# Performance work log

Measured on AMD Instinct MI355X. Metric: run time of the kernel, lower is better.

The kernel has to match this reference:

```python
import jax, jax.numpy as jnp
import numpy as np

DIM = 1024
HIDDEN = 2816  # multiple_of * ceil(int(2*4096/3)/multiple_of)
N_MODALITIES = 2
B, S = 8, 4096


def setup_inputs() -> dict:
    key = jax.random.key(0)
    k_x, k_m, k1, k2, k3 = jax.random.split(key, 5)
    x = jax.random.normal(k_x, (B, S, DIM), dtype=jnp.float32)
    modality_ids = jax.random.randint(k_m, (B, S), 0, N_MODALITIES, dtype=jnp.int32)
    in_std = DIM ** -0.5
    out_std = HIDDEN ** -0.5
    # Linear weight layout: [out_features, in_features], stacked over modalities.
    W1 = jax.random.normal(k1, (N_MODALITIES, HIDDEN, DIM), dtype=jnp.float32) * in_std
    W3 = jax.random.normal(k3, (N_MODALITIES, HIDDEN, DIM), dtype=jnp.float32) * in_std
    W2 = jax.random.normal(k2, (N_MODALITIES, DIM, HIDDEN), dtype=jnp.float32) * out_std
    return {"x": x, "modality_ids": modality_ids, "W1": W1, "W2": W2, "W3": W3}


def reference(x, modality_ids, W1, W2, W3):
    # Masked per-modality SwiGLU; equivalent to gather -> expert MLP -> scatter.
    output = jnp.zeros_like(x)
    for m in range(N_MODALITIES):  # small fixed modality count
        mask = (modality_ids == m)[..., None]          # [B, S, 1]
        x1 = jnp.einsum('bsd,hd->bsh', x, W1[m])       # gate proj
        x3 = jnp.einsum('bsd,hd->bsh', x, W3[m])       # up proj
        out_m = jnp.einsum('bsh,dh->bsd', jax.nn.silu(x1) * x3, W2[m])
        output = output + jnp.where(mask, out_m, 0.0)
    return output
```

## Files before the change

### kernel.cpp

```cpp
#include <hip/hip_runtime.h>
#include <stdint.h>

#define DIMK 1024
#define HID  2816

typedef __attribute__((ext_vector_type(8))) __bf16 bf16x8;
typedef __attribute__((ext_vector_type(4))) float  f32x4;

typedef const __attribute__((address_space(1))) void* gas1_t;
typedef __attribute__((address_space(3))) void*       las3_t;

__device__ __forceinline__ uint16_t f2bf(float f) {
  uint32_t u = __float_as_uint(f);
  u += 0x7FFFu + ((u >> 16) & 1u);
  return (uint16_t)(u >> 16);
}

__device__ __forceinline__ void gload16(const uint16_t* g, uint16_t* l) {
  __builtin_amdgcn_global_load_lds((gas1_t)g, (las3_t)l, 16, 0, 0);
}

template<int N> __device__ __forceinline__ void wait_vm() {
  if constexpr (N == 0)      asm volatile("s_waitcnt vmcnt(0)" ::: "memory");
  else if constexpr (N == 1) asm volatile("s_waitcnt vmcnt(1)" ::: "memory");
  else if constexpr (N == 2) asm volatile("s_waitcnt vmcnt(2)" ::: "memory");
}

__device__ __forceinline__ void stage32(const uint16_t* g, long stride,
                                        uint16_t* lds, int tid) {
  const int row  = tid >> 2;
  const int srcg = (tid & 3) ^ ((tid >> 3) & 3);
  gload16(g + (long)row * stride + srcg * 8, lds + tid * 8);
}

__device__ __forceinline__ bf16x8 ldsf32(const uint16_t* lds, int r, int g) {
  return *reinterpret_cast<const bf16x8*>(lds + r * 32 + ((g ^ ((r >> 1) & 3)) << 3));
}


__global__ void count_kernel(const int* __restrict__ mids, int* __restrict__ bc, int T) {
  const int b = blockIdx.x, t = threadIdx.x;
  const int token = b * 256 + t;
  const int lane = t & 63, wv = t >> 6;
  const int m = (token < T) ? mids[token] : -1;
  unsigned long long m0 = __ballot(m == 0);
  unsigned long long m1 = __ballot(m == 1);
  __shared__ int w0[4], w1[4];
  if (lane == 0) { w0[wv] = __popcll(m0); w1[wv] = __popcll(m1); }
  __syncthreads();
  if (t == 0) {
    bc[2 * b]     = w0[0] + w0[1] + w0[2] + w0[3];
    bc[2 * b + 1] = w1[0] + w1[1] + w1[2] + w1[3];
  }
}

__global__ void scan_kernel(const int* __restrict__ bc, int* __restrict__ base,
                            int* __restrict__ counters, int nb) {
  __shared__ int s0[256], s1[256];
  const int t = threadIdx.x;
  const int v0 = (t < nb) ? bc[2 * t] : 0;
  const int v1 = (t < nb) ? bc[2 * t + 1] : 0;
  s0[t] = v0; s1[t] = v1;
  __syncthreads();
  for (int off = 1; off < 256; off <<= 1) {
    int a0 = (t >= off) ? s0[t - off] : 0;
    int a1 = (t >= off) ? s1[t - off] : 0;
    __syncthreads();
    s0[t] += a0; s1[t] += a1;
    __syncthreads();
  }
  if (t < nb) { base[2 * t] = s0[t] - v0; base[2 * t + 1] = s1[t] - v1; }
  if (t == nb - 1) { counters[0] = s0[t]; counters[1] = s1[t]; }
}

__global__ void slot_kernel(const int* __restrict__ mids, const int* __restrict__ base,
                            const int* __restrict__ counters, int* __restrict__ tok,
                            int* __restrict__ slotof, int T) {
  const int b = blockIdx.x, t = threadIdx.x;
  const int token = b * 256 + t;
  const int lane = t & 63, wv = t >> 6;
  const int m = (token < T) ? mids[token] : -1;
  unsigned long long m0 = __ballot(m == 0);
  unsigned long long m1 = __ballot(m == 1);
  __shared__ int w0[4], w1[4];
  if (lane == 0) { w0[wv] = __popcll(m0); w1[wv] = __popcll(m1); }
  __syncthreads();
  int pre0 = 0, pre1 = 0;
  for (int w = 0; w < wv; ++w) { pre0 += w0[w]; pre1 += w1[w]; }
  if (token >= T) return;
  const unsigned long long below = (1ULL << lane) - 1ULL;
  const int c0 = counters[0];
  const int al0 = ((c0 + 127) >> 7) << 7;
  int slot;
  if (m == 0) slot = base[2 * b] + pre0 + __popcll(m0 & below);
  else        slot = al0 + base[2 * b + 1] + pre1 + __popcll(m1 & below);
  tok[slot] = token;
  slotof[token] = slot;
}

__global__ void copy_kernel(const float* __restrict__ x, const int* __restrict__ slotof,
                            uint16_t* __restrict__ xg, int T) {
  const int token = blockIdx.x * 4 + (threadIdx.x >> 6);
  if (token >= T) return;
  const int lane = threadIdx.x & 63;
  const int slot = slotof[token];
  const float4* src = (const float4*)(x + (long)token * DIMK);
  uint16_t* dst = xg + (long)slot * DIMK;
#pragma unroll
  for (int j = 0; j < 4; ++j) {
    float4 v = src[lane + 64 * j];
    ushort4 o;
    o.x = f2bf(v.x); o.y = f2bf(v.y); o.z = f2bf(v.z); o.w = f2bf(v.w);
    *(ushort4*)(dst + (lane + 64 * j) * 4) = o;
  }
}

__global__ void convert3_kernel(const float* __restrict__ s0, const float* __restrict__ s1,
                                const float* __restrict__ s2, uint16_t* __restrict__ d0,
                                uint16_t* __restrict__ d1, uint16_t* __restrict__ d2,
                                long n, int cblk) {
  const int seg = blockIdx.x / cblk;
  const int bid = blockIdx.x - seg * cblk;
  const float* src = (seg == 0) ? s0 : (seg == 1) ? s1 : s2;
  uint16_t*    dst = (seg == 0) ? d0 : (seg == 1) ? d1 : d2;
  long i = ((long)bid * blockDim.x + threadIdx.x) * 4;
  if (i >= n) return;
  float4 v = *(const float4*)(src + i);
  ushort4 o;
  o.x = f2bf(v.x); o.y = f2bf(v.y); o.z = f2bf(v.z); o.w = f2bf(v.w);
  *(ushort4*)(dst + i) = o;
}


template<bool PF, int W0, int W1>
__device__ __forceinline__ void qt32(
    const uint16_t* Ac, const uint16_t* Bxc, const uint16_t* Byc,
    uint16_t* An, uint16_t* Bxn, uint16_t* Byn,
    const uint16_t* gA, const uint16_t* gBx, const uint16_t* gBy,
    long ko, long stride,
    int tid, int wr, int wc, int lrow, int grp,
    f32x4 (&accX)[4][2], f32x4 (&accY)[4][2]) {
  bf16x8 a[4], bx[2], by[2];
  wait_vm<W0>();
  __builtin_amdgcn_s_barrier();
  asm volatile("" ::: "memory");
#pragma unroll
  for (int m = 0; m < 4; ++m)
    a[m] = ldsf32(Ac, wr * 64 + m * 16 + lrow, grp);
#pragma unroll
  for (int n = 0; n < 2; ++n)
    bx[n] = ldsf32(Bxc, wc * 32 + n * 16 + lrow, grp);
  if constexpr (PF) stage32(gA + ko, stride, An, tid);
  asm volatile("s_waitcnt lgkmcnt(0)" ::: "memory");
  __builtin_amdgcn_sched_barrier(0);
  __builtin_amdgcn_s_setprio(1);
#pragma unroll
  for (int m = 0; m < 4; ++m)
#pragma unroll
    for (int n = 0; n < 2; ++n)
      accX[m][n] = __builtin_amdgcn_mfma_f32_16x16x32_bf16(a[m], bx[n], accX[m][n], 0, 0, 0);
  __builtin_amdgcn_s_setprio(0);
  wait_vm<W1>();
  __builtin_amdgcn_s_barrier();
  asm volatile("" ::: "memory");
#pragma unroll
  for (int n = 0; n < 2; ++n)
    by[n] = ldsf32(Byc, wc * 32 + n * 16 + lrow, grp);
  if constexpr (PF) {
    stage32(gBx + ko, stride, Bxn, tid);
    stage32(gBy + ko, stride, Byn, tid);
  }
  asm volatile("s_waitcnt lgkmcnt(0)" ::: "memory");
  __builtin_amdgcn_sched_barrier(0);
  __builtin_amdgcn_s_setprio(1);
#pragma unroll
  for (int m = 0; m < 4; ++m)
#pragma unroll
    for (int n = 0; n < 2; ++n)
      accY[m][n] = __builtin_amdgcn_mfma_f32_16x16x32_bf16(a[m], by[n], accY[m][n], 0, 0, 0);
  __builtin_amdgcn_s_setprio(0);
}


__global__ __launch_bounds__(512, 4) void gemm1_kernel(
    const uint16_t* __restrict__ xg, const uint16_t* __restrict__ w1b,
    const uint16_t* __restrict__ w3b, uint16_t* __restrict__ hbuf,
    const int* __restrict__ counters) {
  __shared__ __align__(16) uint16_t lsA[2][128 * 32];
  __shared__ __align__(16) uint16_t lsB1[2][128 * 32];
  __shared__ __align__(16) uint16_t lsB3[2][128 * 32];

  const int c0 = counters[0], c1 = counters[1];
  const int t0 = (c0 + 127) >> 7, t1 = (c1 + 127) >> 7;
  const int NHT = gridDim.y;
  const int nwg = gridDim.x * NHT;
  const int orig = blockIdx.y * gridDim.x + blockIdx.x;
  const int q = nwg >> 3, r = nwg & 7;
  const int xcd = orig & 7, loc = orig >> 3;
  const int swz = (xcd < r ? xcd * (q + 1) : r * (q + 1) + (xcd - r) * q) + loc;
  const int rt = swz / NHT;
  const int ht = swz - rt * NHT;
  if (rt >= t0 + t1) return;
  const int mod = (rt < t0) ? 0 : 1;
  const long row0 = (long)rt * 128;

  const int tid = threadIdx.x, lane = tid & 63, wv = tid >> 6;
  const int wr = wv >> 2, wc = wv & 3;
  const int lrow = lane & 15, grp = lane >> 4;

  const uint16_t* gA  = xg  + row0 * DIMK;
  const uint16_t* gB1 = w1b + ((long)mod * HID + ht * 128) * DIMK;
  const uint16_t* gB3 = w3b + ((long)mod * HID + ht * 128) * DIMK;

  f32x4 accG[4][2], accU[4][2];
#pragma unroll
  for (int m = 0; m < 4; ++m)
#pragma unroll
    for (int n = 0; n < 2; ++n) {
      accG[m][n] = {0.f, 0.f, 0.f, 0.f};
      accU[m][n] = {0.f, 0.f, 0.f, 0.f};
    }

  stage32(gA,  DIMK, &lsA[0][0],  tid);
  stage32(gB1, DIMK, &lsB1[0][0], tid);
  stage32(gB3, DIMK, &lsB3[0][0], tid);

  const int NT = DIMK / 32;
  int cur = 0;
  for (int t = 0; t < NT - 1; ++t) {
    qt32<true, 1, 1>(&lsA[cur][0], &lsB1[cur][0], &lsB3[cur][0],
                     &lsA[cur ^ 1][0], &lsB1[cur ^ 1][0], &lsB3[cur ^ 1][0],
                     gA, gB1, gB3, (long)(t + 1) * 32, DIMK,
                     tid, wr, wc, lrow, grp, accG, accU);
    cur ^= 1;
  }
  qt32<false, 1, 0>(&lsA[cur][0], &lsB1[cur][0], &lsB3[cur][0],
                    &lsA[cur ^ 1][0], &lsB1[cur ^ 1][0], &lsB3[cur ^ 1][0],
                    gA, gB1, gB3, 0, DIMK,
                    tid, wr, wc, lrow, grp, accG, accU);

#pragma unroll
  for (int m = 0; m < 4; ++m)
#pragma unroll
    for (int n = 0; n < 2; ++n) {
      const int col = ht * 128 + wc * 32 + n * 16 + lrow;
#pragma unroll
      for (int i = 0; i < 4; ++i) {
        const long row = row0 + wr * 64 + m * 16 + grp * 4 + i;
        float g = accG[m][n][i];
        float u = accU[m][n][i];
        float hv = (g / (1.f + __expf(-g))) * u;
        hbuf[row * HID + col] = f2bf(hv);
      }
    }
}


__global__ __launch_bounds__(512, 4) void gemm2_kernel(
    const uint16_t* __restrict__ hbuf, const uint16_t* __restrict__ w2b,
    const int* __restrict__ counters, const int* __restrict__ tok,
    float* __restrict__ out) {
  __shared__ __align__(16) uint16_t lsA[2][128 * 32];
  __shared__ __align__(16) uint16_t lsBx[2][128 * 32];
  __shared__ __align__(16) uint16_t lsBy[2][128 * 32];

  const int c0 = counters[0], c1 = counters[1];
  const int t0 = (c0 + 127) >> 7, t1 = (c1 + 127) >> 7;
  const int NCT = gridDim.y;
  const int nwg = gridDim.x * NCT;
  const int orig = blockIdx.y * gridDim.x + blockIdx.x;
  const int q = nwg >> 3, r = nwg & 7;
  const int xcd = orig & 7, loc = orig >> 3;
  const int swz = (xcd < r ? xcd * (q + 1) : r * (q + 1) + (xcd - r) * q) + loc;
  const int rt = swz / NCT;
  const int ct = swz - rt * NCT;
  if (rt >= t0 + t1) return;
  const int mod = (rt < t0) ? 0 : 1;
  const long row0 = (long)rt * 128;
  const int vlimit = (mod == 0) ? c0 : t0 * 128 + c1;

  const int tid = threadIdx.x, lane = tid & 63, wv = tid >> 6;
  const int wr = wv >> 2, wc = wv & 3;
  const int lrow = lane & 15, grp = lane >> 4;

  const uint16_t* gA  = hbuf + row0 * HID;
  const uint16_t* gBx = w2b + ((long)mod * DIMK + ct * 256) * HID;
  const uint16_t* gBy = gBx + 128 * HID;

  f32x4 accX[4][2], accY[4][2];
#pragma unroll
  for (int m = 0; m < 4; ++m)
#pragma unroll
    for (int n = 0; n < 2; ++n) {
      accX[m][n] = {0.f, 0.f, 0.f, 0.f};
      accY[m][n] = {0.f, 0.f, 0.f, 0.f};
    }

  stage32(gA,  HID, &lsA[0][0],  tid);
  stage32(gBx, HID, &lsBx[0][0], tid);
  stage32(gBy, HID, &lsBy[0][0], tid);

  const int NT = HID / 32;
  int cur = 0;
  for (int t = 0; t < NT - 1; ++t) {
    qt32<true, 1, 1>(&lsA[cur][0], &lsBx[cur][0], &lsBy[cur][0],
                     &lsA[cur ^ 1][0], &lsBx[cur ^ 1][0], &lsBy[cur ^ 1][0],
                     gA, gBx, gBy, (long)(t + 1) * 32, HID,
                     tid, wr, wc, lrow, grp, accX, accY);
    cur ^= 1;
  }
  qt32<false, 1, 0>(&lsA[cur][0], &lsBx[cur][0], &lsBy[cur][0],
                    &lsA[cur ^ 1][0], &lsBx[cur ^ 1][0], &lsBy[cur ^ 1][0],
                    gA, gBx, gBy, 0, HID,
                    tid, wr, wc, lrow, grp, accX, accY);

#pragma unroll
  for (int m = 0; m < 4; ++m)
#pragma unroll
    for (int n = 0; n < 2; ++n) {
      const int colX = ct * 256 + wc * 32 + n * 16 + lrow;
#pragma unroll
      for (int i = 0; i < 4; ++i) {
        const int row = (int)row0 + wr * 64 + m * 16 + grp * 4 + i;
        if (row < vlimit) {
          const long obase = (long)tok[row] * DIMK;
          out[obase + colX]       = accX[m][n][i];
          out[obase + colX + 128] = accY[m][n][i];
        }
      }
    }
}

extern "C" void kernel_launch(void* const* d_in, const int* in_sizes, int n_in,
                              void* d_out, int out_size, void* d_ws, size_t ws_size,
                              hipStream_t stream) {
  const float* x    = (const float*)d_in[0];
  const int*   mids = (const int*)d_in[1];
  const float* W1   = (const float*)d_in[2];
  const float* W2   = (const float*)d_in[3];
  const float* W3   = (const float*)d_in[4];
  float* out = (float*)d_out;

  const int T   = in_sizes[1];
  const int NB  = (T + 255) / 256;
  const int CAP = ((T + 127) & ~127) + 128;

  char* ws = (char*)d_ws;
  int* counters = (int*)ws;
  int* bc   = (int*)(ws + 256);
  int* base = (int*)(ws + 256 + 2048);
  int* tok  = (int*)(ws + 256 + 4096);
  int* slotof = tok + ((CAP + 63) & ~63);
  size_t off = 256 + 4096 + (size_t)((CAP + 63) & ~63) * 4 + (size_t)((T + 63) & ~63) * 4;
  off = (off + 255) & ~(size_t)255;
  uint16_t* xg  = (uint16_t*)(ws + off); off += (size_t)CAP * DIMK * 2;
  uint16_t* w1b = (uint16_t*)(ws + off); off += (size_t)2 * HID * DIMK * 2;
  uint16_t* w3b = (uint16_t*)(ws + off); off += (size_t)2 * HID * DIMK * 2;
  uint16_t* w2b = (uint16_t*)(ws + off); off += (size_t)2 * DIMK * HID * 2;
  uint16_t* hbuf = (uint16_t*)(ws + off); off += (size_t)CAP * HID * 2;
  (void)ws_size; (void)n_in; (void)out_size;

  count_kernel<<<NB, 256, 0, stream>>>(mids, bc, T);
  scan_kernel<<<1, 256, 0, stream>>>(bc, base, counters, NB);
  slot_kernel<<<NB, 256, 0, stream>>>(mids, base, counters, tok, slotof, T);
  copy_kernel<<<(T + 3) / 4, 256, 0, stream>>>(x, slotof, xg, T);

  const long NW = (long)2 * HID * DIMK;
  const int cblk = (int)((NW / 4 + 255) / 256);
  convert3_kernel<<<3 * cblk, 256, 0, stream>>>(W1, W3, W2, w1b, w3b, w2b, NW, cblk);

  const int rtiles = CAP / 128;
  gemm1_kernel<<<dim3(rtiles, HID / 128), 512, 0, stream>>>(xg, w1b, w3b, hbuf, counters);
  gemm2_kernel<<<dim3(rtiles, DIMK / 256), 512, 0, stream>>>(hbuf, w2b, counters, tok, out);
}
```

Before: 724.6 us.

## Deepen LDS pipeline to triple buffering in both GEMM kernels

Switches both grouped GEMM kernels from double to triple LDS buffering, prefetching two K-slices ahead and relaxing the vmcnt waits so more global loads stay in flight. The aim is to hide global-to-LDS latency behind MFMA work. In exchange LDS use per block grows from 48KB to 72KB, which may lower the number of resident blocks per CU relative to the launch bound of 4.

```diff
diff --git a/kernel.cpp b/kernel.cpp
--- a/kernel.cpp
+++ b/kernel.cpp
@@ -23,7 +23,8 @@
 template<int N> __device__ __forceinline__ void wait_vm() {
   if constexpr (N == 0)      asm volatile("s_waitcnt vmcnt(0)" ::: "memory");
   else if constexpr (N == 1) asm volatile("s_waitcnt vmcnt(1)" ::: "memory");
-  else if constexpr (N == 2) asm volatile("s_waitcnt vmcnt(2)" ::: "memory");
+  else if constexpr (N == 3) asm volatile("s_waitcnt vmcnt(3)" ::: "memory");
+  else if constexpr (N == 4) asm volatile("s_waitcnt vmcnt(4)" ::: "memory");
 }
 
 __device__ __forceinline__ void stage32(const uint16_t* g, long stride,
@@ -186,9 +187,9 @@
     const uint16_t* __restrict__ xg, const uint16_t* __restrict__ w1b,
     const uint16_t* __restrict__ w3b, uint16_t* __restrict__ hbuf,
     const int* __restrict__ counters) {
-  __shared__ __align__(16) uint16_t lsA[2][128 * 32];
-  __shared__ __align__(16) uint16_t lsB1[2][128 * 32];
-  __shared__ __align__(16) uint16_t lsB3[2][128 * 32];
+  __shared__ __align__(16) uint16_t lsA[3][128 * 32];
+  __shared__ __align__(16) uint16_t lsB1[3][128 * 32];
+  __shared__ __align__(16) uint16_t lsB3[3][128 * 32];
 
   const int c0 = counters[0], c1 = counters[1];
   const int t0 = (c0 + 127) >> 7, t1 = (c1 + 127) >> 7;
@@ -221,21 +222,30 @@
       accU[m][n] = {0.f, 0.f, 0.f, 0.f};
     }
 
-  stage32(gA,  DIMK, &lsA[0][0],  tid);
-  stage32(gB1, DIMK, &lsB1[0][0], tid);
-  stage32(gB3, DIMK, &lsB3[0][0], tid);
+  stage32(gA,        DIMK, &lsA[0][0],  tid);
+  stage32(gB1,       DIMK, &lsB1[0][0], tid);
+  stage32(gB3,       DIMK, &lsB3[0][0], tid);
+  stage32(gA + 32,   DIMK, &lsA[1][0],  tid);
+  stage32(gB1 + 32,  DIMK, &lsB1[1][0], tid);
+  stage32(gB3 + 32,  DIMK, &lsB3[1][0], tid);
 
   const int NT = DIMK / 32;
   int cur = 0;
-  for (int t = 0; t < NT - 1; ++t) {
-    qt32<true, 1, 1>(&lsA[cur][0], &lsB1[cur][0], &lsB3[cur][0],
-                     &lsA[cur ^ 1][0], &lsB1[cur ^ 1][0], &lsB3[cur ^ 1][0],
-                     gA, gB1, gB3, (long)(t + 1) * 32, DIMK,
+  for (int t = 0; t < NT - 2; ++t) {
+    const int nx2 = (cur + 2) % 3;
+    qt32<true, 4, 4>(&lsA[cur][0], &lsB1[cur][0], &lsB3[cur][0],
+                     &lsA[nx2][0], &lsB1[nx2][0], &lsB3[nx2][0],
+                     gA, gB1, gB3, (long)(t + 2) * 32, DIMK,
                      tid, wr, wc, lrow, grp, accG, accU);
-    cur ^= 1;
-  }
+    cur = (cur + 1) % 3;
+  }
+  qt32<false, 4, 3>(&lsA[cur][0], &lsB1[cur][0], &lsB3[cur][0],
+                    &lsA[cur][0], &lsB1[cur][0], &lsB3[cur][0],
+                    gA, gB1, gB3, 0, DIMK,
+                    tid, wr, wc, lrow, grp, accG, accU);
+  cur = (cur + 1) % 3;
   qt32<false, 1, 0>(&lsA[cur][0], &lsB1[cur][0], &lsB3[cur][0],
-                    &lsA[cur ^ 1][0], &lsB1[cur ^ 1][0], &lsB3[cur ^ 1][0],
+                    &lsA[cur][0], &lsB1[cur][0], &lsB3[cur][0],
                     gA, gB1, gB3, 0, DIMK,
                     tid, wr, wc, lrow, grp, accG, accU);
 
@@ -260,9 +270,9 @@
     const uint16_t* __restrict__ hbuf, const uint16_t* __restrict__ w2b,
     const int* __restrict__ counters, const int* __restrict__ tok,
     float* __restrict__ out) {
-  __shared__ __align__(16) uint16_t lsA[2][128 * 32];
-  __shared__ __align__(16) uint16_t lsBx[2][128 * 32];
-  __shared__ __align__(16) uint16_t lsBy[2][128 * 32];
+  __shared__ __align__(16) uint16_t lsA[3][128 * 32];
+  __shared__ __align__(16) uint16_t lsBx[3][128 * 32];
+  __shared__ __align__(16) uint16_t lsBy[3][128 * 32];
 
   const int c0 = counters[0], c1 = counters[1];
   const int t0 = (c0 + 127) >> 7, t1 = (c1 + 127) >> 7;
@@ -296,21 +306,30 @@
       accY[m][n] = {0.f, 0.f, 0.f, 0.f};
     }
 
-  stage32(gA,  HID, &lsA[0][0],  tid);
-  stage32(gBx, HID, &lsBx[0][0], tid);
-  stage32(gBy, HID, &lsBy[0][0], tid);
+  stage32(gA,        HID, &lsA[0][0],  tid);
+  stage32(gBx,       HID, &lsBx[0][0], tid);
+  stage32(gBy,       HID, &lsBy[0][0], tid);
+  stage32(gA + 32,   HID, &lsA[1][0],  tid);
+  stage32(gBx + 32,  HID, &lsBx[1][0], tid);
+  stage32(gBy + 32,  HID, &lsBy[1][0], tid);
 
   const int NT = HID / 32;
   int cur = 0;
-  for (int t = 0; t < NT - 1; ++t) {
-    qt32<true, 1, 1>(&lsA[cur][0], &lsBx[cur][0], &lsBy[cur][0],
-                     &lsA[cur ^ 1][0], &lsBx[cur ^ 1][0], &lsBy[cur ^ 1][0],
-                     gA, gBx, gBy, (long)(t + 1) * 32, HID,
+  for (int t = 0; t < NT - 2; ++t) {
+    const int nx2 = (cur + 2) % 3;
+    qt32<true, 4, 4>(&lsA[cur][0], &lsBx[cur][0], &lsBy[cur][0],
+                     &lsA[nx2][0], &lsBx[nx2][0], &lsBy[nx2][0],
+                     gA, gBx, gBy, (long)(t + 2) * 32, HID,
                      tid, wr, wc, lrow, grp, accX, accY);
-    cur ^= 1;
-  }
+    cur = (cur + 1) % 3;
+  }
+  qt32<false, 4, 3>(&lsA[cur][0], &lsBx[cur][0], &lsBy[cur][0],
+                    &lsA[cur][0], &lsBx[cur][0], &lsBy[cur][0],
+                    gA, gBx, gBy, 0, HID,
+                    tid, wr, wc, lrow, grp, accX, accY);
+  cur = (cur + 1) % 3;
   qt32<false, 1, 0>(&lsA[cur][0], &lsBx[cur][0], &lsBy[cur][0],
-                    &lsA[cur ^ 1][0], &lsBx[cur ^ 1][0], &lsBy[cur ^ 1][0],
+                    &lsA[cur][0], &lsBx[cur][0], &lsBy[cur][0],
                     gA, gBx, gBy, 0, HID,
                     tid, wr, wc, lrow, grp, accX, accY);
 
```

After: 726.8 us. About the same (+0.3%).
